# Kernel optimization log

Hardware: AMD Instinct MI355X
Metric: run time of the kernel (lower is better)

## Reference

```python
import jax, jax.numpy as jnp
import numpy as np

NUM_EXPERTS = 8
TOP_K = 2
ROUTED_SCALE = 1.0  # routed_scaling_factor
D_MODEL = 2048
D_FFN = 1408


def setup_inputs() -> dict:
    key = jax.random.key(0)
    ks = jax.random.split(key, 8)
    s = 0.02  # init scale for weights
    return {
        'hidden_states': jax.random.normal(ks[0], (2, 1024, D_MODEL), jnp.float32),
        'gate_w': jax.random.normal(ks[1], (NUM_EXPERTS, D_MODEL), jnp.float32) * s,
        'w_gate': jax.random.normal(ks[2], (NUM_EXPERTS, D_MODEL, D_FFN), jnp.float32) * s,
        'w_up': jax.random.normal(ks[3], (NUM_EXPERTS, D_MODEL, D_FFN), jnp.float32) * s,
        'w_down': jax.random.normal(ks[4], (NUM_EXPERTS, D_FFN, D_MODEL), jnp.float32) * s,
        'sw_gate': jax.random.normal(ks[5], (D_MODEL, D_FFN), jnp.float32) * s,
        'sw_up': jax.random.normal(ks[6], (D_MODEL, D_FFN), jnp.float32) * s,
        'sw_down': jax.random.normal(ks[7], (D_FFN, D_MODEL), jnp.float32) * s,
    }


def reference(hidden_states, gate_w, w_gate, w_up, w_down, sw_gate, sw_up, sw_down):
    B, S, D = hidden_states.shape
    x = hidden_states.reshape(-1, D)            # [T, D]
    T = x.shape[0]

    # --- router: fp32 linear -> softmax -> top-k -> renormalize ---
    logits = jnp.einsum('td,ed->te', x.astype(jnp.float32), gate_w)   # [T, E]
    probs = jax.nn.softmax(logits, axis=-1)
    topk_w, topk_ids = jax.lax.top_k(probs, TOP_K)                    # [T, K]
    topk_w = topk_w / jnp.sum(topk_w, axis=-1, keepdims=True)         # norm_topk_prob
    # dense per-token expert gates [T, E] (zero for unselected experts)
    gates = jnp.zeros((T, NUM_EXPERTS), jnp.float32).at[
        jnp.arange(T)[:, None], topk_ids].add(topk_w)
    gates = gates.astype(x.dtype)

    # --- routed experts: SwiGLU per expert, masked dense combine ---
    g = jnp.einsum('td,edf->etf', x, w_gate)    # [E, T, F]
    u = jnp.einsum('td,edf->etf', x, w_up)      # [E, T, F]
    h = jax.nn.silu(g) * u                      # SiluAndMul
    down = jnp.einsum('etf,efd->etd', h, w_down)  # [E, T, D]
    routed = jnp.einsum('te,etd->td', gates, down)  # combine
    routed = routed * ROUTED_SCALE

    # --- shared expert MLP ---
    shared = (jax.nn.silu(x @ sw_gate) * (x @ sw_up)) @ sw_down

    out = routed + shared
    return out.reshape(B, S, D)
```

## Files before the change

kernel.cpp:

```cpp
#include <hip/hip_runtime.h>
#include <hip/hip_bf16.h>

#define T_TOK 2048
#define DM    2048
#define FF    1408
#define NE    8
#define MT_ROUTED 40
#define MT_TOTAL  56
#define ROUTED_CAP 5120
#define NSLOT 7168

typedef unsigned short u16;
typedef __attribute__((ext_vector_type(4))) u16 u16x4;
typedef __attribute__((ext_vector_type(8))) short bf16x8;
typedef __attribute__((ext_vector_type(4))) float f32x4;

__device__ __forceinline__ u16 f2bf(float f) {
    unsigned u = __float_as_uint(f);
    unsigned r = (u + 0x7FFFu + ((u >> 16) & 1u)) >> 16;
    return (u16)r;
}
__device__ __forceinline__ float bf2f(u16 v) {
    return __uint_as_float(((unsigned)v) << 16);
}

__device__ __forceinline__ void gll16(const void* g, void* l) {
    __builtin_amdgcn_global_load_lds((const __attribute__((address_space(1))) void*)g,
                                     (__attribute__((address_space(3))) void*)l, 16, 0, 0);
}

constexpr size_t SZ_XB  = (size_t)T_TOK * DM * 2;
constexpr size_t SZ_WE  = (size_t)NE * DM * FF * 2;
constexpr size_t SZ_SW  = (size_t)DM * FF * 2;
constexpr size_t SZ_H   = (size_t)NSLOT * FF * 2;
constexpr size_t SZ_DN  = (size_t)NSLOT * DM * 2;

constexpr size_t OFF_XB   = 0;
constexpr size_t OFF_WGT  = OFF_XB + SZ_XB;
constexpr size_t OFF_WUT  = OFF_WGT + SZ_WE;
constexpr size_t OFF_WDT  = OFF_WUT + SZ_WE;
constexpr size_t OFF_SWG  = OFF_WDT + SZ_WE;
constexpr size_t OFF_SWU  = OFF_SWG + SZ_SW;
constexpr size_t OFF_SWD  = OFF_SWU + SZ_SW;
constexpr size_t OFF_H    = OFF_SWD + SZ_SW;
constexpr size_t OFF_DN   = OFF_H + SZ_H;
constexpr size_t OFF_TID  = OFF_DN + SZ_DN;
constexpr size_t OFF_TW   = OFF_TID + (size_t)T_TOK*2*4;
constexpr size_t OFF_PERM = OFF_TW  + (size_t)T_TOK*2*4;
constexpr size_t OFF_SW_S = OFF_PERM + (size_t)ROUTED_CAP*4;
constexpr size_t OFF_TKS  = OFF_SW_S + (size_t)ROUTED_CAP*4;
constexpr size_t OFF_TE   = OFF_TKS + (size_t)T_TOK*2*4;

__global__ void tcvtA_kernel(const float* __restrict__ wg, const float* __restrict__ wu,
                             const float* __restrict__ swg, const float* __restrict__ swu,
                             u16* __restrict__ wgT, u16* __restrict__ wuT,
                             u16* __restrict__ swgT, u16* __restrict__ swuT) {
    __shared__ u16 tile[64][72];
    const int z = blockIdx.z;
    const size_t msz = (size_t)DM * FF;
    const float* s; u16* d;
    if (z < 8)       { s = wg + (size_t)z * msz;        d = wgT + (size_t)z * msz; }
    else if (z < 16) { s = wu + (size_t)(z - 8) * msz;  d = wuT + (size_t)(z - 8) * msz; }
    else if (z == 16){ s = swg;                          d = swgT; }
    else             { s = swu;                          d = swuT; }
    const int R = DM, C = FF;
    const int r0 = blockIdx.y * 64, c0 = blockIdx.x * 64;
    const int tr = threadIdx.x >> 4, tc = (threadIdx.x & 15) * 4;
#pragma unroll
    for (int i = 0; i < 4; i++) {
        const int r = tr + i * 16;
        const float4 v = *(const float4*)(s + (size_t)(r0 + r) * C + (c0 + tc));
        tile[r][tc+0] = f2bf(v.x); tile[r][tc+1] = f2bf(v.y);
        tile[r][tc+2] = f2bf(v.z); tile[r][tc+3] = f2bf(v.w);
    }
    __syncthreads();
#pragma unroll
    for (int i = 0; i < 4; i++) {
        const int c = tr + i * 16;
        u16x4 o;
        o.x = tile[tc+0][c]; o.y = tile[tc+1][c]; o.z = tile[tc+2][c]; o.w = tile[tc+3][c];
        *(u16x4*)(d + (size_t)(c0 + c) * R + (r0 + tc)) = o;
    }
}

__global__ void tcvtB_kernel(const float* __restrict__ wd, const float* __restrict__ swd,
                             u16* __restrict__ wdT, u16* __restrict__ swdT) {
    __shared__ u16 tile[64][72];
    const int z = blockIdx.z;
    const size_t msz = (size_t)DM * FF;
    const float* s; u16* d;
    if (z < 8) { s = wd + (size_t)z * msz; d = wdT + (size_t)z * msz; }
    else       { s = swd;                  d = swdT; }
    const int R = FF, C = DM;
    const int r0 = blockIdx.y * 64, c0 = blockIdx.x * 64;
    const int tr = threadIdx.x >> 4, tc = (threadIdx.x & 15) * 4;
#pragma unroll
    for (int i = 0; i < 4; i++) {
        const int r = tr + i * 16;
        const float4 v = *(const float4*)(s + (size_t)(r0 + r) * C + (c0 + tc));
        tile[r][tc+0] = f2bf(v.x); tile[r][tc+1] = f2bf(v.y);
        tile[r][tc+2] = f2bf(v.z); tile[r][tc+3] = f2bf(v.w);
    }
    __syncthreads();
#pragma unroll
    for (int i = 0; i < 4; i++) {
        const int c = tr + i * 16;
        u16x4 o;
        o.x = tile[tc+0][c]; o.y = tile[tc+1][c]; o.z = tile[tc+2][c]; o.w = tile[tc+3][c];
        *(u16x4*)(d + (size_t)(c0 + c) * R + (r0 + tc)) = o;
    }
}

__global__ void router_kernel(const float* __restrict__ x, const float* __restrict__ gw,
                              u16* __restrict__ xb,
                              int* __restrict__ topk_id, float* __restrict__ topk_w) {
    const int wv = threadIdx.x >> 6, l = threadIdx.x & 63;
    const int t = blockIdx.x * 4 + wv;
    const float* xt = x + (size_t)t * DM;
    u16* xbt = xb + (size_t)t * DM;
    float acc[NE] = {0.f,0.f,0.f,0.f,0.f,0.f,0.f,0.f};
    for (int d = l * 4; d < DM; d += 256) {
        const float4 xv = *(const float4*)(xt + d);
        u16x4 o; o.x = f2bf(xv.x); o.y = f2bf(xv.y); o.z = f2bf(xv.z); o.w = f2bf(xv.w);
        *(u16x4*)(xbt + d) = o;
#pragma unroll
        for (int e = 0; e < NE; e++) {
            const float4 w4 = *(const float4*)(gw + e * DM + d);
            acc[e] += xv.x * w4.x + xv.y * w4.y + xv.z * w4.z + xv.w * w4.w;
        }
    }
#pragma unroll
    for (int e = 0; e < NE; e++)
#pragma unroll
        for (int off = 32; off > 0; off >>= 1) acc[e] += __shfl_xor(acc[e], off, 64);
    if (l == 0) {
        float m = acc[0];
#pragma unroll
        for (int e = 1; e < NE; e++) m = fmaxf(m, acc[e]);
        float p[NE];
#pragma unroll
        for (int e = 0; e < NE; e++) p[e] = __expf(acc[e] - m);
        int i1 = 0; float b1 = p[0];
#pragma unroll
        for (int e = 1; e < NE; e++) if (p[e] > b1) { b1 = p[e]; i1 = e; }
        int i2 = -1; float b2 = -1.f;
#pragma unroll
        for (int e = 0; e < NE; e++) if (e != i1 && p[e] > b2) { b2 = p[e]; i2 = e; }
        const float s = b1 + b2;
        topk_id[2*t] = i1; topk_id[2*t+1] = i2;
        topk_w[2*t] = b1 / s; topk_w[2*t+1] = b2 / s;
    }
}

__global__ void scan_kernel(const int* __restrict__ topk_id, const float* __restrict__ topk_w,
                            int* __restrict__ perm_token, float* __restrict__ slot_w,
                            int* __restrict__ tk_slot, int* __restrict__ tile_e) {
    const int e = blockIdx.x;
    const int tid = threadIdx.x;
    __shared__ int cnt[NE];
    __shared__ int tsum[256];
    int ids[16];
#pragma unroll
    for (int j = 0; j < 16; j++) ids[j] = topk_id[tid * 16 + j];
    if (tid < NE) cnt[tid] = 0;
    __syncthreads();
#pragma unroll
    for (int e2 = 0; e2 < NE; e2++) {
        int c = 0;
#pragma unroll
        for (int j = 0; j < 16; j++) c += (ids[j] == e2);
        if (c) atomicAdd(&cnt[e2], c);
    }
    int mySum = 0;
#pragma unroll
    for (int j = 0; j < 16; j++) mySum += (ids[j] == e);
    tsum[tid] = mySum;
    __syncthreads();
    if (tid == 0) { int run = 0; for (int i = 0; i < 256; i++) { int v = tsum[i]; tsum[i] = run; run += v; } }
    __syncthreads();
    int poff = 0;
#pragma unroll
    for (int e2 = 0; e2 < NE; e2++) { int p = (cnt[e2] + 127) & ~127; if (e2 < e) poff += p; }
    const int padded_e = (cnt[e] + 127) & ~127;
    int run = tsum[tid];
#pragma unroll
    for (int j = 0; j < 16; j++) {
        if (ids[j] == e) {
            const int i = tid * 16 + j;
            const int slot = poff + run;
            perm_token[slot] = i >> 1;
            slot_w[slot] = topk_w[i];
            tk_slot[i] = slot;
            run++;
        }
    }
    for (int r = cnt[e] + tid; r < padded_e; r += 256) { perm_token[poff + r] = 0; slot_w[poff + r] = 0.f; }
    if (tid == 0) for (int tt = poff >> 7; tt < (poff + padded_e) >> 7; tt++) tile_e[tt] = e;
    if (e == 0 && tid == 1) {
        int ptot = 0;
#pragma unroll
        for (int e2 = 0; e2 < NE; e2++) ptot += (cnt[e2] + 127) & ~127;
        for (int tt = ptot >> 7; tt < MT_ROUTED; tt++) tile_e[tt] = -1;
        for (int tt = MT_ROUTED; tt < MT_TOTAL; tt++) tile_e[tt] = 8;
    }
}

__global__ __launch_bounds__(256, 3)
void gemm1_kernel(const u16* __restrict__ xb,
                  const u16* __restrict__ wgT, const u16* __restrict__ wuT,
                  const u16* __restrict__ swgT, const u16* __restrict__ swuT,
                  const int* __restrict__ perm_token, const float* __restrict__ slot_w,
                  const int* __restrict__ tile_e, u16* __restrict__ hbuf) {
    const int mtile = blockIdx.y, ntile = blockIdx.x;
    const int e = tile_e[mtile];
    if (e < 0) return;
    __shared__ u16 lA[128 * 64], lB[128 * 64];
    __shared__ int lTok[128];
    __shared__ float lW[128];
    const int tid = threadIdx.x, l = tid & 63, w = tid >> 6;
    const bool sh = (e == 8);
    const int slot_base = sh ? (ROUTED_CAP + (mtile - MT_ROUTED) * 128) : mtile * 128;
    if (tid < 128) {
        if (sh) { lTok[tid] = (mtile - MT_ROUTED) * 128 + tid; lW[tid] = 1.0f; }
        else {
            int tok = perm_token[slot_base + tid];
            lTok[tid] = (tok < 0) ? 0 : tok;
            lW[tid] = slot_w[slot_base + tid];
        }
    }
    __syncthreads();
    const u16* Bg = sh ? swgT : (wgT + (size_t)e * FF * DM);
    const u16* Bu = sh ? swuT : (wuT + (size_t)e * FF * DM);
    const int n0 = ntile * 64;
    const u16* aSrc[4]; const u16* bSrc[4]; int ldsOff[4];
#pragma unroll
    for (int i = 0; i < 4; i++) {
        const int row = i * 32 + w * 8 + (l >> 3);
        const int ch = (l & 7) ^ (row & 7);
        ldsOff[i] = (i * 32 + w * 8) * 64;
        aSrc[i] = xb + (size_t)lTok[row] * DM + ch * 8;
        const u16* bbase = (i < 2) ? (Bg + (size_t)(n0 + row) * DM)
                                   : (Bu + (size_t)(n0 + row - 64) * DM);
        bSrc[i] = bbase + ch * 8;
    }
    f32x4 acc[2][8] = {};
    const int wm = w * 32;
    for (int k0 = 0; k0 < DM; k0 += 64) {
        __syncthreads();
#pragma unroll
        for (int i = 0; i < 4; i++) { gll16(aSrc[i] + k0, lA + ldsOff[i]); gll16(bSrc[i] + k0, lB + ldsOff[i]); }
        __syncthreads();
#pragma unroll
        for (int kk = 0; kk < 64; kk += 32) {
            bf16x8 af[2], bf_[8];
#pragma unroll
            for (int mi = 0; mi < 2; mi++) {
                const int row = wm + mi * 16 + (l & 15);
                const int ch = ((kk >> 3) + (l >> 4)) ^ (row & 7);
                af[mi] = *(const bf16x8*)(lA + row * 64 + ch * 8);
            }
#pragma unroll
            for (int ni = 0; ni < 8; ni++) {
                const int row = ni * 16 + (l & 15);
                const int ch = ((kk >> 3) + (l >> 4)) ^ (row & 7);
                bf_[ni] = *(const bf16x8*)(lB + row * 64 + ch * 8);
            }
#pragma unroll
            for (int mi = 0; mi < 2; mi++)
#pragma unroll
                for (int ni = 0; ni < 8; ni++)
                    acc[mi][ni] = __builtin_amdgcn_mfma_f32_16x16x32_bf16(af[mi], bf_[ni], acc[mi][ni], 0, 0, 0);
        }
    }
#pragma unroll
    for (int mi = 0; mi < 2; mi++)
#pragma unroll
        for (int r = 0; r < 4; r++) {
            const int m = wm + mi * 16 + (l >> 4) * 4 + r;
            const float wgt = lW[m];
#pragma unroll
            for (int ni = 0; ni < 4; ni++) {
                const int n = ni * 16 + (l & 15);
                const float g = acc[mi][ni][r], u = acc[mi][ni + 4][r];
                const float h = g * (1.f / (1.f + __expf(-g))) * u * wgt;
                hbuf[(size_t)(slot_base + m) * FF + n0 + n] = f2bf(h);
            }
        }
}

__global__ __launch_bounds__(256, 4)
void gemm2_kernel(const u16* __restrict__ hbuf, const u16* __restrict__ wdT,
                  const u16* __restrict__ swdT, const int* __restrict__ tile_e,
                  u16* __restrict__ dn) {
    const int mtile = blockIdx.y, ntile = blockIdx.x;
    const int e = tile_e[mtile];
    if (e < 0) return;
    __shared__ u16 lA[128 * 64], lB[64 * 64];
    const int tid = threadIdx.x, l = tid & 63, w = tid >> 6;
    const bool sh = (e == 8);
    const int slot_base = sh ? (ROUTED_CAP + (mtile - MT_ROUTED) * 128) : mtile * 128;
    const u16* Bp = sh ? swdT : (wdT + (size_t)e * DM * FF);
    const int n0 = ntile * 64;
    const u16* aSrc[4]; const u16* bSrc[2]; int ldsOffA[4]; int ldsOffB[2];
#pragma unroll
    for (int i = 0; i < 4; i++) {
        const int row = i * 32 + w * 8 + (l >> 3);
        const int ch = (l & 7) ^ (row & 7);
        ldsOffA[i] = (i * 32 + w * 8) * 64;
        aSrc[i] = hbuf + (size_t)(slot_base + row) * FF + ch * 8;
    }
#pragma unroll
    for (int i = 0; i < 2; i++) {
        const int row = i * 32 + w * 8 + (l >> 3);
        const int ch = (l & 7) ^ (row & 7);
        ldsOffB[i] = (i * 32 + w * 8) * 64;
        bSrc[i] = Bp + (size_t)(n0 + row) * FF + ch * 8;
    }
    f32x4 acc[2][4] = {};
    const int wm = w * 32;
    for (int k0 = 0; k0 < FF; k0 += 64) {
        __syncthreads();
#pragma unroll
        for (int i = 0; i < 4; i++) gll16(aSrc[i] + k0, lA + ldsOffA[i]);
#pragma unroll
        for (int i = 0; i < 2; i++) gll16(bSrc[i] + k0, lB + ldsOffB[i]);
        __syncthreads();
#pragma unroll
        for (int kk = 0; kk < 64; kk += 32) {
            bf16x8 af[2], bf_[4];
#pragma unroll
            for (int mi = 0; mi < 2; mi++) {
                const int row = wm + mi * 16 + (l & 15);
                const int ch = ((kk >> 3) + (l >> 4)) ^ (row & 7);
                af[mi] = *(const bf16x8*)(lA + row * 64 + ch * 8);
            }
#pragma unroll
            for (int ni = 0; ni < 4; ni++) {
                const int row = ni * 16 + (l & 15);
                const int ch = ((kk >> 3) + (l >> 4)) ^ (row & 7);
                bf_[ni] = *(const bf16x8*)(lB + row * 64 + ch * 8);
            }
#pragma unroll
            for (int mi = 0; mi < 2; mi++)
#pragma unroll
                for (int ni = 0; ni < 4; ni++)
                    acc[mi][ni] = __builtin_amdgcn_mfma_f32_16x16x32_bf16(af[mi], bf_[ni], acc[mi][ni], 0, 0, 0);
        }
    }
#pragma unroll
    for (int mi = 0; mi < 2; mi++)
#pragma unroll
        for (int r = 0; r < 4; r++) {
            const int m = wm + mi * 16 + (l >> 4) * 4 + r;
#pragma unroll
            for (int ni = 0; ni < 4; ni++) {
                const int n = ni * 16 + (l & 15);
                dn[(size_t)(slot_base + m) * DM + n0 + n] = f2bf(acc[mi][ni][r]);
            }
        }
}

__global__ void combine_kernel(const u16* __restrict__ dn, const int* __restrict__ tk_slot,
                               float* __restrict__ out) {
    const int i = blockIdx.x * 256 + threadIdx.x;
    const int base = i * 8;
    const int t = base >> 11, d = base & 2047;
    const int s1 = tk_slot[2 * t], s2 = tk_slot[2 * t + 1];
    const bf16x8 a = *(const bf16x8*)(dn + (size_t)s1 * DM + d);
    const bf16x8 b = *(const bf16x8*)(dn + (size_t)s2 * DM + d);
    const bf16x8 c = *(const bf16x8*)(dn + (size_t)(ROUTED_CAP + t) * DM + d);
    float o[8];
#pragma unroll
    for (int j = 0; j < 8; j++)
        o[j] = bf2f((u16)a[j]) + bf2f((u16)b[j]) + bf2f((u16)c[j]);
    float4 lo, hi;
    lo.x = o[0]; lo.y = o[1]; lo.z = o[2]; lo.w = o[3];
    hi.x = o[4]; hi.y = o[5]; hi.z = o[6]; hi.w = o[7];
    *(float4*)(out + base) = lo;
    *(float4*)(out + base + 4) = hi;
}

extern "C" void kernel_launch(void* const* d_in, const int* in_sizes, int n_in,
                              void* d_out, int out_size, void* d_ws, size_t ws_size,
                              hipStream_t stream) {
    (void)in_sizes; (void)n_in; (void)out_size; (void)ws_size;
    const float* x   = (const float*)d_in[0];
    const float* gw  = (const float*)d_in[1];
    const float* wg  = (const float*)d_in[2];
    const float* wu  = (const float*)d_in[3];
    const float* wd  = (const float*)d_in[4];
    const float* swg = (const float*)d_in[5];
    const float* swu = (const float*)d_in[6];
    const float* swd = (const float*)d_in[7];
    float* out = (float*)d_out;
    char* ws = (char*)d_ws;

    u16*   xb    = (u16*)(ws + OFF_XB);
    u16*   wgT   = (u16*)(ws + OFF_WGT);
    u16*   wuT   = (u16*)(ws + OFF_WUT);
    u16*   wdT   = (u16*)(ws + OFF_WDT);
    u16*   swgT  = (u16*)(ws + OFF_SWG);
    u16*   swuT  = (u16*)(ws + OFF_SWU);
    u16*   swdT  = (u16*)(ws + OFF_SWD);
    u16*   hbuf  = (u16*)(ws + OFF_H);
    u16*   dn    = (u16*)(ws + OFF_DN);
    int*   tid_  = (int*)(ws + OFF_TID);
    float* tw    = (float*)(ws + OFF_TW);
    int*   perm  = (int*)(ws + OFF_PERM);
    float* slw   = (float*)(ws + OFF_SW_S);
    int*   tks   = (int*)(ws + OFF_TKS);
    int*   te    = (int*)(ws + OFF_TE);

    router_kernel<<<T_TOK / 4, 256, 0, stream>>>(x, gw, xb, tid_, tw);
    scan_kernel<<<NE, 256, 0, stream>>>(tid_, tw, perm, slw, tks, te);
    tcvtA_kernel<<<dim3(FF / 64, DM / 64, 18), 256, 0, stream>>>(wg, wu, swg, swu, wgT, wuT, swgT, swuT);
    tcvtB_kernel<<<dim3(DM / 64, FF / 64, 9), 256, 0, stream>>>(wd, swd, wdT, swdT);
    gemm1_kernel<<<dim3(FF / 64, MT_TOTAL), 256, 0, stream>>>(xb, wgT, wuT, swgT, swuT, perm, slw, te, hbuf);
    gemm2_kernel<<<dim3(DM / 64, MT_TOTAL), 256, 0, stream>>>(hbuf, wdT, swdT, te, dn);
    combine_kernel<<<(T_TOK * DM / 8) / 256, 256, 0, stream>>>(dn, tks, out);
}
```

Before: 293.4 us.

## Enlarge GEMM M-tiles to 256 rows with 512-thread blocks and 2D warp split

Expert-sorted token tiles are padded to 256 rows instead of 128, and both GEMM kernels now run 512-thread blocks with a 2D warp layout. GEMM2 also widens its N tile to 128. The larger tiles cut how often weights are reloaded per token and raise MFMA work per LDS load. In exchange there is more padding waste per expert, fewer blocks in the grid (possibly under-filling the CUs), and more LDS and register pressure per block.

After: 401.6 us. +36.9%, slower.

```diff
diff --git a/kernel.cpp b/kernel.cpp
--- a/kernel.cpp
+++ b/kernel.cpp
@@ -5,10 +5,11 @@
 #define DM    2048
 #define FF    1408
 #define NE    8
-#define MT_ROUTED 40
-#define MT_TOTAL  56
-#define ROUTED_CAP 5120
-#define NSLOT 7168
+#define BMT   256
+#define MT_ROUTED 24
+#define MT_TOTAL  32
+#define ROUTED_CAP 6144
+#define NSLOT 8192
 
 typedef unsigned short u16;
 typedef __attribute__((ext_vector_type(4))) u16 u16x4;
@@ -180,8 +181,8 @@
     __syncthreads();
     int poff = 0;
 #pragma unroll
-    for (int e2 = 0; e2 < NE; e2++) { int p = (cnt[e2] + 127) & ~127; if (e2 < e) poff += p; }
-    const int padded_e = (cnt[e] + 127) & ~127;
+    for (int e2 = 0; e2 < NE; e2++) { int p = (cnt[e2] + 255) & ~255; if (e2 < e) poff += p; }
+    const int padded_e = (cnt[e] + 255) & ~255;
     int run = tsum[tid];
 #pragma unroll
     for (int j = 0; j < 16; j++) {
@@ -195,17 +196,17 @@
         }
     }
     for (int r = cnt[e] + tid; r < padded_e; r += 256) { perm_token[poff + r] = 0; slot_w[poff + r] = 0.f; }
-    if (tid == 0) for (int tt = poff >> 7; tt < (poff + padded_e) >> 7; tt++) tile_e[tt] = e;
+    if (tid == 0) for (int tt = poff >> 8; tt < (poff + padded_e) >> 8; tt++) tile_e[tt] = e;
     if (e == 0 && tid == 1) {
         int ptot = 0;
 #pragma unroll
-        for (int e2 = 0; e2 < NE; e2++) ptot += (cnt[e2] + 127) & ~127;
-        for (int tt = ptot >> 7; tt < MT_ROUTED; tt++) tile_e[tt] = -1;
+        for (int e2 = 0; e2 < NE; e2++) ptot += (cnt[e2] + 255) & ~255;
+        for (int tt = ptot >> 8; tt < MT_ROUTED; tt++) tile_e[tt] = -1;
         for (int tt = MT_ROUTED; tt < MT_TOTAL; tt++) tile_e[tt] = 8;
     }
 }
 
-__global__ __launch_bounds__(256, 3)
+__global__ __launch_bounds__(512, 4)
 void gemm1_kernel(const u16* __restrict__ xb,
                   const u16* __restrict__ wgT, const u16* __restrict__ wuT,
                   const u16* __restrict__ swgT, const u16* __restrict__ swuT,
@@ -214,147 +215,154 @@
     const int mtile = blockIdx.y, ntile = blockIdx.x;
     const int e = tile_e[mtile];
     if (e < 0) return;
-    __shared__ u16 lA[128 * 64], lB[128 * 64];
-    __shared__ int lTok[128];
-    __shared__ float lW[128];
+    __shared__ u16 lA[256 * 64], lB[128 * 64];
+    __shared__ int lTok[256];
+    __shared__ float lW[256];
     const int tid = threadIdx.x, l = tid & 63, w = tid >> 6;
     const bool sh = (e == 8);
-    const int slot_base = sh ? (ROUTED_CAP + (mtile - MT_ROUTED) * 128) : mtile * 128;
-    if (tid < 128) {
-        if (sh) { lTok[tid] = (mtile - MT_ROUTED) * 128 + tid; lW[tid] = 1.0f; }
-        else {
-            int tok = perm_token[slot_base + tid];
-            lTok[tid] = (tok < 0) ? 0 : tok;
-            lW[tid] = slot_w[slot_base + tid];
-        }
+    const int slot_base = sh ? (ROUTED_CAP + (mtile - MT_ROUTED) * BMT) : mtile * BMT;
+    if (tid < 256) {
+        if (sh) { lTok[tid] = (mtile - MT_ROUTED) * BMT + tid; lW[tid] = 1.0f; }
+        else    { lTok[tid] = perm_token[slot_base + tid]; lW[tid] = slot_w[slot_base + tid]; }
     }
     __syncthreads();
     const u16* Bg = sh ? swgT : (wgT + (size_t)e * FF * DM);
     const u16* Bu = sh ? swuT : (wuT + (size_t)e * FF * DM);
     const int n0 = ntile * 64;
-    const u16* aSrc[4]; const u16* bSrc[4]; int ldsOff[4];
-#pragma unroll
-    for (int i = 0; i < 4; i++) {
-        const int row = i * 32 + w * 8 + (l >> 3);
+    const u16* aSrc[4]; const u16* bSrc[2]; int aOff[4], bOff[2];
+#pragma unroll
+    for (int i = 0; i < 4; i++) {
+        const int row = i * 64 + w * 8 + (l >> 3);
         const int ch = (l & 7) ^ (row & 7);
-        ldsOff[i] = (i * 32 + w * 8) * 64;
+        aOff[i] = (i * 64 + w * 8) * 64;
         aSrc[i] = xb + (size_t)lTok[row] * DM + ch * 8;
-        const u16* bbase = (i < 2) ? (Bg + (size_t)(n0 + row) * DM)
-                                   : (Bu + (size_t)(n0 + row - 64) * DM);
+    }
+#pragma unroll
+    for (int i = 0; i < 2; i++) {
+        const int row = i * 64 + w * 8 + (l >> 3);
+        const int ch = (l & 7) ^ (row & 7);
+        bOff[i] = (i * 64 + w * 8) * 64;
+        const u16* bbase = (i == 0) ? (Bg + (size_t)(n0 + row) * DM)
+                                    : (Bu + (size_t)(n0 + row - 64) * DM);
         bSrc[i] = bbase + ch * 8;
     }
-    f32x4 acc[2][8] = {};
-    const int wm = w * 32;
+    f32x4 accg[4][2] = {}; f32x4 accu[4][2] = {};
+    const int wm = (w >> 1) * 64, wn = (w & 1) * 32;
     for (int k0 = 0; k0 < DM; k0 += 64) {
         __syncthreads();
 #pragma unroll
-        for (int i = 0; i < 4; i++) { gll16(aSrc[i] + k0, lA + ldsOff[i]); gll16(bSrc[i] + k0, lB + ldsOff[i]); }
+        for (int i = 0; i < 4; i++) gll16(aSrc[i] + k0, lA + aOff[i]);
+#pragma unroll
+        for (int i = 0; i < 2; i++) gll16(bSrc[i] + k0, lB + bOff[i]);
         __syncthreads();
 #pragma unroll
         for (int kk = 0; kk < 64; kk += 32) {
-            bf16x8 af[2], bf_[8];
-#pragma unroll
-            for (int mi = 0; mi < 2; mi++) {
+            bf16x8 af[4], bgf[2], buf2[2];
+#pragma unroll
+            for (int mi = 0; mi < 4; mi++) {
                 const int row = wm + mi * 16 + (l & 15);
                 const int ch = ((kk >> 3) + (l >> 4)) ^ (row & 7);
                 af[mi] = *(const bf16x8*)(lA + row * 64 + ch * 8);
             }
 #pragma unroll
-            for (int ni = 0; ni < 8; ni++) {
-                const int row = ni * 16 + (l & 15);
-                const int ch = ((kk >> 3) + (l >> 4)) ^ (row & 7);
-                bf_[ni] = *(const bf16x8*)(lB + row * 64 + ch * 8);
-            }
-#pragma unroll
-            for (int mi = 0; mi < 2; mi++)
-#pragma unroll
-                for (int ni = 0; ni < 8; ni++)
-                    acc[mi][ni] = __builtin_amdgcn_mfma_f32_16x16x32_bf16(af[mi], bf_[ni], acc[mi][ni], 0, 0, 0);
-        }
-    }
-#pragma unroll
-    for (int mi = 0; mi < 2; mi++)
+            for (int ni = 0; ni < 2; ni++) {
+                const int rowg = wn + ni * 16 + (l & 15);
+                const int ch = ((kk >> 3) + (l >> 4)) ^ (rowg & 7);
+                bgf[ni]  = *(const bf16x8*)(lB + rowg * 64 + ch * 8);
+                buf2[ni] = *(const bf16x8*)(lB + (rowg + 64) * 64 + ch * 8);
+            }
+#pragma unroll
+            for (int mi = 0; mi < 4; mi++)
+#pragma unroll
+                for (int ni = 0; ni < 2; ni++) {
+                    accg[mi][ni] = __builtin_amdgcn_mfma_f32_16x16x32_bf16(af[mi], bgf[ni], accg[mi][ni], 0, 0, 0);
+                    accu[mi][ni] = __builtin_amdgcn_mfma_f32_16x16x32_bf16(af[mi], buf2[ni], accu[mi][ni], 0, 0, 0);
+                }
+        }
+    }
+#pragma unroll
+    for (int mi = 0; mi < 4; mi++)
 #pragma unroll
         for (int r = 0; r < 4; r++) {
             const int m = wm + mi * 16 + (l >> 4) * 4 + r;
             const float wgt = lW[m];
 #pragma unroll
-            for (int ni = 0; ni < 4; ni++) {
-                const int n = ni * 16 + (l & 15);
-                const float g = acc[mi][ni][r], u = acc[mi][ni + 4][r];
+            for (int ni = 0; ni < 2; ni++) {
+                const int n = wn + ni * 16 + (l & 15);
+                const float g = accg[mi][ni][r], u = accu[mi][ni][r];
                 const float h = g * (1.f / (1.f + __expf(-g))) * u * wgt;
                 hbuf[(size_t)(slot_base + m) * FF + n0 + n] = f2bf(h);
             }
         }
 }
 
-__global__ __launch_bounds__(256, 4)
+__global__ __launch_bounds__(512, 4)
 void gemm2_kernel(const u16* __restrict__ hbuf, const u16* __restrict__ wdT,
                   const u16* __restrict__ swdT, const int* __restrict__ tile_e,
                   u16* __restrict__ dn) {
     const int mtile = blockIdx.y, ntile = blockIdx.x;
     const int e = tile_e[mtile];
     if (e < 0) return;
-    __shared__ u16 lA[128 * 64], lB[64 * 64];
+    __shared__ u16 lA[256 * 64], lB[128 * 64];
     const int tid = threadIdx.x, l = tid & 63, w = tid >> 6;
     const bool sh = (e == 8);
-    const int slot_base = sh ? (ROUTED_CAP + (mtile - MT_ROUTED) * 128) : mtile * 128;
+    const int slot_base = sh ? (ROUTED_CAP + (mtile - MT_ROUTED) * BMT) : mtile * BMT;
     const u16* Bp = sh ? swdT : (wdT + (size_t)e * DM * FF);
-    const int n0 = ntile * 64;
-    const u16* aSrc[4]; const u16* bSrc[2]; int ldsOffA[4]; int ldsOffB[2];
-#pragma unroll
-    for (int i = 0; i < 4; i++) {
-        const int row = i * 32 + w * 8 + (l >> 3);
+    const int n0 = ntile * 128;
+    const u16* aSrc[4]; const u16* bSrc[2]; int aOff[4], bOff[2];
+#pragma unroll
+    for (int i = 0; i < 4; i++) {
+        const int row = i * 64 + w * 8 + (l >> 3);
         const int ch = (l & 7) ^ (row & 7);
-        ldsOffA[i] = (i * 32 + w * 8) * 64;
+        aOff[i] = (i * 64 + w * 8) * 64;
         aSrc[i] = hbuf + (size_t)(slot_base + row) * FF + ch * 8;
     }
 #pragma unroll
     for (int i = 0; i < 2; i++) {
-        const int row = i * 32 + w * 8 + (l >> 3);
+        const int row = i * 64 + w * 8 + (l >> 3);
         const int ch = (l & 7) ^ (row & 7);
-        ldsOffB[i] = (i * 32 + w * 8) * 64;
+        bOff[i] = (i * 64 + w * 8) * 64;
         bSrc[i] = Bp + (size_t)(n0 + row) * FF + ch * 8;
     }
-    f32x4 acc[2][4] = {};
-    const int wm = w * 32;
+    f32x4 acc[4][4] = {};
+    const int wm = (w >> 1) * 64, wn = (w & 1) * 64;
     for (int k0 = 0; k0 < FF; k0 += 64) {
         __syncthreads();
 #pragma unroll
-        for (int i = 0; i < 4; i++) gll16(aSrc[i] + k0, lA + ldsOffA[i]);
-#pragma unroll
-        for (int i = 0; i < 2; i++) gll16(bSrc[i] + k0, lB + ldsOffB[i]);
+        for (int i = 0; i < 4; i++) gll16(aSrc[i] + k0, lA + aOff[i]);
+#pragma unroll
+        for (int i = 0; i < 2; i++) gll16(bSrc[i] + k0, lB + bOff[i]);
         __syncthreads();
 #pragma unroll
         for (int kk = 0; kk < 64; kk += 32) {
-            bf16x8 af[2], bf_[4];
-#pragma unroll
-            for (int mi = 0; mi < 2; mi++) {
+            bf16x8 af[4], bf_[4];
+#pragma unroll
+            for (int mi = 0; mi < 4; mi++) {
                 const int row = wm + mi * 16 + (l & 15);
                 const int ch = ((kk >> 3) + (l >> 4)) ^ (row & 7);
                 af[mi] = *(const bf16x8*)(lA + row * 64 + ch * 8);
             }
 #pragma unroll
             for (int ni = 0; ni < 4; ni++) {
-                const int row = ni * 16 + (l & 15);
+                const int row = wn + ni * 16 + (l & 15);
                 const int ch = ((kk >> 3) + (l >> 4)) ^ (row & 7);
                 bf_[ni] = *(const bf16x8*)(lB + row * 64 + ch * 8);
             }
 #pragma unroll
-            for (int mi = 0; mi < 2; mi++)
+            for (int mi = 0; mi < 4; mi++)
 #pragma unroll
                 for (int ni = 0; ni < 4; ni++)
                     acc[mi][ni] = __builtin_amdgcn_mfma_f32_16x16x32_bf16(af[mi], bf_[ni], acc[mi][ni], 0, 0, 0);
         }
     }
 #pragma unroll
-    for (int mi = 0; mi < 2; mi++)
+    for (int mi = 0; mi < 4; mi++)
 #pragma unroll
         for (int r = 0; r < 4; r++) {
             const int m = wm + mi * 16 + (l >> 4) * 4 + r;
 #pragma unroll
             for (int ni = 0; ni < 4; ni++) {
-                const int n = ni * 16 + (l & 15);
+                const int n = wn + ni * 16 + (l & 15);
                 dn[(size_t)(slot_base + m) * DM + n0 + n] = f2bf(acc[mi][ni][r]);
             }
         }
@@ -415,7 +423,7 @@
     scan_kernel<<<NE, 256, 0, stream>>>(tid_, tw, perm, slw, tks, te);
     tcvtA_kernel<<<dim3(FF / 64, DM / 64, 18), 256, 0, stream>>>(wg, wu, swg, swu, wgT, wuT, swgT, swuT);
     tcvtB_kernel<<<dim3(DM / 64, FF / 64, 9), 256, 0, stream>>>(wd, swd, wdT, swdT);
-    gemm1_kernel<<<dim3(FF / 64, MT_TOTAL), 256, 0, stream>>>(xb, wgT, wuT, swgT, swuT, perm, slw, te, hbuf);
-    gemm2_kernel<<<dim3(DM / 64, MT_TOTAL), 256, 0, stream>>>(hbuf, wdT, swdT, te, dn);
+    gemm1_kernel<<<dim3(FF / 64, MT_TOTAL), 512, 0, stream>>>(xb, wgT, wuT, swgT, swuT, perm, slw, te, hbuf);
+    gemm2_kernel<<<dim3(DM / 128, MT_TOTAL), 512, 0, stream>>>(hbuf, wdT, swdT, te, dn);
     combine_kernel<<<(T_TOK * DM / 8) / 256, 256, 0, stream>>>(dn, tks, out);
 }
```

## Double-buffer GEMM LDS tiles, swizzle block order, merge weight transpose kernels

Applied to the files above, without the earlier changes.

Both expert GEMMs now keep two LDS buffers and prefetch the next K-slice with async global-to-LDS loads while computing the current one, replacing the two-barrier load-then-compute loop. Blocks get a 1-D launch with an XCD-aware swizzle so tiles sharing a weight slice land together. The two weight transpose/convert kernels become one launch. The cost is doubled LDS, lower occupancy bounds, and a dropped guard on negative token indices.

Result: slower. 343.7 us (+17.1%).

```diff
diff --git a/kernel.cpp b/kernel.cpp
--- a/kernel.cpp
+++ b/kernel.cpp
@@ -51,48 +51,30 @@
 constexpr size_t OFF_TKS  = OFF_SW_S + (size_t)ROUTED_CAP*4;
 constexpr size_t OFF_TE   = OFF_TKS + (size_t)T_TOK*2*4;
 
-__global__ void tcvtA_kernel(const float* __restrict__ wg, const float* __restrict__ wu,
-                             const float* __restrict__ swg, const float* __restrict__ swu,
-                             u16* __restrict__ wgT, u16* __restrict__ wuT,
-                             u16* __restrict__ swgT, u16* __restrict__ swuT) {
+__global__ void tcvt_kernel(const float* __restrict__ wg, const float* __restrict__ wu,
+                            const float* __restrict__ swg, const float* __restrict__ swu,
+                            const float* __restrict__ wd, const float* __restrict__ swd,
+                            u16* __restrict__ wgT, u16* __restrict__ wuT,
+                            u16* __restrict__ swgT, u16* __restrict__ swuT,
+                            u16* __restrict__ wdT, u16* __restrict__ swdT) {
     __shared__ u16 tile[64][72];
     const int z = blockIdx.z;
     const size_t msz = (size_t)DM * FF;
-    const float* s; u16* d;
-    if (z < 8)       { s = wg + (size_t)z * msz;        d = wgT + (size_t)z * msz; }
-    else if (z < 16) { s = wu + (size_t)(z - 8) * msz;  d = wuT + (size_t)(z - 8) * msz; }
-    else if (z == 16){ s = swg;                          d = swgT; }
-    else             { s = swu;                          d = swuT; }
-    const int R = DM, C = FF;
-    const int r0 = blockIdx.y * 64, c0 = blockIdx.x * 64;
-    const int tr = threadIdx.x >> 4, tc = (threadIdx.x & 15) * 4;
-#pragma unroll
-    for (int i = 0; i < 4; i++) {
-        const int r = tr + i * 16;
-        const float4 v = *(const float4*)(s + (size_t)(r0 + r) * C + (c0 + tc));
-        tile[r][tc+0] = f2bf(v.x); tile[r][tc+1] = f2bf(v.y);
-        tile[r][tc+2] = f2bf(v.z); tile[r][tc+3] = f2bf(v.w);
-    }
-    __syncthreads();
-#pragma unroll
-    for (int i = 0; i < 4; i++) {
-        const int c = tr + i * 16;
-        u16x4 o;
-        o.x = tile[tc+0][c]; o.y = tile[tc+1][c]; o.z = tile[tc+2][c]; o.w = tile[tc+3][c];
-        *(u16x4*)(d + (size_t)(c0 + c) * R + (r0 + tc)) = o;
-    }
-}
-
-__global__ void tcvtB_kernel(const float* __restrict__ wd, const float* __restrict__ swd,
-                             u16* __restrict__ wdT, u16* __restrict__ swdT) {
-    __shared__ u16 tile[64][72];
-    const int z = blockIdx.z;
-    const size_t msz = (size_t)DM * FF;
-    const float* s; u16* d;
-    if (z < 8) { s = wd + (size_t)z * msz; d = wdT + (size_t)z * msz; }
-    else       { s = swd;                  d = swdT; }
-    const int R = FF, C = DM;
-    const int r0 = blockIdx.y * 64, c0 = blockIdx.x * 64;
+    const float* s; u16* d; int R, C, trow, tcol;
+    if (z < 18) {
+        R = DM; C = FF;
+        trow = blockIdx.x / 22; tcol = blockIdx.x % 22;
+        if (z < 8)       { s = wg + (size_t)z * msz;       d = wgT + (size_t)z * msz; }
+        else if (z < 16) { s = wu + (size_t)(z - 8) * msz; d = wuT + (size_t)(z - 8) * msz; }
+        else if (z == 16){ s = swg;                         d = swgT; }
+        else             { s = swu;                         d = swuT; }
+    } else {
+        R = FF; C = DM;
+        trow = blockIdx.x / 32; tcol = blockIdx.x % 32;
+        if (z < 26) { s = wd + (size_t)(z - 18) * msz; d = wdT + (size_t)(z - 18) * msz; }
+        else        { s = swd;                          d = swdT; }
+    }
+    const int r0 = trow * 64, c0 = tcol * 64;
     const int tr = threadIdx.x >> 4, tc = (threadIdx.x & 15) * 4;
 #pragma unroll
     for (int i = 0; i < 4; i++) {
@@ -205,16 +187,18 @@
     }
 }
 
-__global__ __launch_bounds__(256, 3)
+__global__ __launch_bounds__(256, 2)
 void gemm1_kernel(const u16* __restrict__ xb,
                   const u16* __restrict__ wgT, const u16* __restrict__ wuT,
                   const u16* __restrict__ swgT, const u16* __restrict__ swuT,
                   const int* __restrict__ perm_token, const float* __restrict__ slot_w,
                   const int* __restrict__ tile_e, u16* __restrict__ hbuf) {
-    const int mtile = blockIdx.y, ntile = blockIdx.x;
+    const int bid = blockIdx.x;
+    const int swz = (bid & 7) * 154 + (bid >> 3);
+    const int mtile = swz % 56, ntile = swz / 56;
     const int e = tile_e[mtile];
     if (e < 0) return;
-    __shared__ u16 lA[128 * 64], lB[128 * 64];
+    __shared__ u16 lA[2][128 * 64], lB[2][128 * 64];
     __shared__ int lTok[128];
     __shared__ float lW[128];
     const int tid = threadIdx.x, l = tid & 63, w = tid >> 6;
@@ -222,11 +206,7 @@
     const int slot_base = sh ? (ROUTED_CAP + (mtile - MT_ROUTED) * 128) : mtile * 128;
     if (tid < 128) {
         if (sh) { lTok[tid] = (mtile - MT_ROUTED) * 128 + tid; lW[tid] = 1.0f; }
-        else {
-            int tok = perm_token[slot_base + tid];
-            lTok[tid] = (tok < 0) ? 0 : tok;
-            lW[tid] = slot_w[slot_base + tid];
-        }
+        else    { lTok[tid] = perm_token[slot_base + tid]; lW[tid] = slot_w[slot_base + tid]; }
     }
     __syncthreads();
     const u16* Bg = sh ? swgT : (wgT + (size_t)e * FF * DM);
@@ -245,11 +225,15 @@
     }
     f32x4 acc[2][8] = {};
     const int wm = w * 32;
-    for (int k0 = 0; k0 < DM; k0 += 64) {
-        __syncthreads();
-#pragma unroll
-        for (int i = 0; i < 4; i++) { gll16(aSrc[i] + k0, lA + ldsOff[i]); gll16(bSrc[i] + k0, lB + ldsOff[i]); }
-        __syncthreads();
+
+    auto stage = [&](int buf, int k0) {
+#pragma unroll
+        for (int i = 0; i < 4; i++) {
+            gll16(aSrc[i] + k0, lA[buf] + ldsOff[i]);
+            gll16(bSrc[i] + k0, lB[buf] + ldsOff[i]);
+        }
+    };
+    auto compute = [&](int buf) {
 #pragma unroll
         for (int kk = 0; kk < 64; kk += 32) {
             bf16x8 af[2], bf_[8];
@@ -257,13 +241,13 @@
             for (int mi = 0; mi < 2; mi++) {
                 const int row = wm + mi * 16 + (l & 15);
                 const int ch = ((kk >> 3) + (l >> 4)) ^ (row & 7);
-                af[mi] = *(const bf16x8*)(lA + row * 64 + ch * 8);
+                af[mi] = *(const bf16x8*)(lA[buf] + row * 64 + ch * 8);
             }
 #pragma unroll
             for (int ni = 0; ni < 8; ni++) {
                 const int row = ni * 16 + (l & 15);
                 const int ch = ((kk >> 3) + (l >> 4)) ^ (row & 7);
-                bf_[ni] = *(const bf16x8*)(lB + row * 64 + ch * 8);
+                bf_[ni] = *(const bf16x8*)(lB[buf] + row * 64 + ch * 8);
             }
 #pragma unroll
             for (int mi = 0; mi < 2; mi++)
@@ -271,7 +255,21 @@
                 for (int ni = 0; ni < 8; ni++)
                     acc[mi][ni] = __builtin_amdgcn_mfma_f32_16x16x32_bf16(af[mi], bf_[ni], acc[mi][ni], 0, 0, 0);
         }
-    }
+    };
+
+    stage(0, 0);
+    for (int t = 0; t < 31; t++) {
+        const int cur = t & 1;
+        stage(cur ^ 1, (t + 1) * 64);
+        asm volatile("s_waitcnt vmcnt(8)" ::: "memory");
+        __builtin_amdgcn_s_barrier();
+        compute(cur);
+        __builtin_amdgcn_s_barrier();
+    }
+    asm volatile("s_waitcnt vmcnt(0)" ::: "memory");
+    __builtin_amdgcn_s_barrier();
+    compute(1);
+
 #pragma unroll
     for (int mi = 0; mi < 2; mi++)
 #pragma unroll
@@ -288,43 +286,46 @@
         }
 }
 
-__global__ __launch_bounds__(256, 4)
+__global__ __launch_bounds__(256, 3)
 void gemm2_kernel(const u16* __restrict__ hbuf, const u16* __restrict__ wdT,
                   const u16* __restrict__ swdT, const int* __restrict__ tile_e,
                   u16* __restrict__ dn) {
-    const int mtile = blockIdx.y, ntile = blockIdx.x;
+    const int bid = blockIdx.x;
+    const int swz = (bid & 7) * 224 + (bid >> 3);
+    const int mtile = swz % 56, ntile = swz / 56;
     const int e = tile_e[mtile];
     if (e < 0) return;
-    __shared__ u16 lA[128 * 64], lB[64 * 64];
+    __shared__ u16 lA[2][128 * 64], lB[2][64 * 64];
     const int tid = threadIdx.x, l = tid & 63, w = tid >> 6;
     const bool sh = (e == 8);
     const int slot_base = sh ? (ROUTED_CAP + (mtile - MT_ROUTED) * 128) : mtile * 128;
     const u16* Bp = sh ? swdT : (wdT + (size_t)e * DM * FF);
     const int n0 = ntile * 64;
-    const u16* aSrc[4]; const u16* bSrc[2]; int ldsOffA[4]; int ldsOffB[2];
+    const u16* aSrc[4]; const u16* bSrc[2]; int aOff[4], bOff[2];
 #pragma unroll
     for (int i = 0; i < 4; i++) {
         const int row = i * 32 + w * 8 + (l >> 3);
         const int ch = (l & 7) ^ (row & 7);
-        ldsOffA[i] = (i * 32 + w * 8) * 64;
+        aOff[i] = (i * 32 + w * 8) * 64;
         aSrc[i] = hbuf + (size_t)(slot_base + row) * FF + ch * 8;
     }
 #pragma unroll
     for (int i = 0; i < 2; i++) {
         const int row = i * 32 + w * 8 + (l >> 3);
         const int ch = (l & 7) ^ (row & 7);
-        ldsOffB[i] = (i * 32 + w * 8) * 64;
+        bOff[i] = (i * 32 + w * 8) * 64;
         bSrc[i] = Bp + (size_t)(n0 + row) * FF + ch * 8;
     }
     f32x4 acc[2][4] = {};
     const int wm = w * 32;
-    for (int k0 = 0; k0 < FF; k0 += 64) {
-        __syncthreads();
-#pragma unroll
-        for (int i = 0; i < 4; i++) gll16(aSrc[i] + k0, lA + ldsOffA[i]);
-#pragma unroll
-        for (int i = 0; i < 2; i++) gll16(bSrc[i] + k0, lB + ldsOffB[i]);
-        __syncthreads();
+
+    auto stage = [&](int buf, int k0) {
+#pragma unroll
+        for (int i = 0; i < 4; i++) gll16(aSrc[i] + k0, lA[buf] + aOff[i]);
+#pragma unroll
+        for (int i = 0; i < 2; i++) gll16(bSrc[i] + k0, lB[buf] + bOff[i]);
+    };
+    auto compute = [&](int buf) {
 #pragma unroll
         for (int kk = 0; kk < 64; kk += 32) {
             bf16x8 af[2], bf_[4];
@@ -332,13 +333,13 @@
             for (int mi = 0; mi < 2; mi++) {
                 const int row = wm + mi * 16 + (l & 15);
                 const int ch = ((kk >> 3) + (l >> 4)) ^ (row & 7);
-                af[mi] = *(const bf16x8*)(lA + row * 64 + ch * 8);
+                af[mi] = *(const bf16x8*)(lA[buf] + row * 64 + ch * 8);
             }
 #pragma unroll
             for (int ni = 0; ni < 4; ni++) {
                 const int row = ni * 16 + (l & 15);
                 const int ch = ((kk >> 3) + (l >> 4)) ^ (row & 7);
-                bf_[ni] = *(const bf16x8*)(lB + row * 64 + ch * 8);
+                bf_[ni] = *(const bf16x8*)(lB[buf] + row * 64 + ch * 8);
             }
 #pragma unroll
             for (int mi = 0; mi < 2; mi++)
@@ -346,7 +347,21 @@
                 for (int ni = 0; ni < 4; ni++)
                     acc[mi][ni] = __builtin_amdgcn_mfma_f32_16x16x32_bf16(af[mi], bf_[ni], acc[mi][ni], 0, 0, 0);
         }
-    }
+    };
+
+    stage(0, 0);
+    for (int t = 0; t < 21; t++) {
+        const int cur = t & 1;
+        stage(cur ^ 1, (t + 1) * 64);
+        asm volatile("s_waitcnt vmcnt(6)" ::: "memory");
+        __builtin_amdgcn_s_barrier();
+        compute(cur);
+        __builtin_amdgcn_s_barrier();
+    }
+    asm volatile("s_waitcnt vmcnt(0)" ::: "memory");
+    __builtin_amdgcn_s_barrier();
+    compute(1);
+
 #pragma unroll
     for (int mi = 0; mi < 2; mi++)
 #pragma unroll
@@ -413,9 +428,9 @@
 
     router_kernel<<<T_TOK / 4, 256, 0, stream>>>(x, gw, xb, tid_, tw);
     scan_kernel<<<NE, 256, 0, stream>>>(tid_, tw, perm, slw, tks, te);
-    tcvtA_kernel<<<dim3(FF / 64, DM / 64, 18), 256, 0, stream>>>(wg, wu, swg, swu, wgT, wuT, swgT, swuT);
-    tcvtB_kernel<<<dim3(DM / 64, FF / 64, 9), 256, 0, stream>>>(wd, swd, wdT, swdT);
-    gemm1_kernel<<<dim3(FF / 64, MT_TOTAL), 256, 0, stream>>>(xb, wgT, wuT, swgT, swuT, perm, slw, te, hbuf);
-    gemm2_kernel<<<dim3(DM / 64, MT_TOTAL), 256, 0, stream>>>(hbuf, wdT, swdT, te, dn);
+    tcvt_kernel<<<dim3(704, 1, 27), 256, 0, stream>>>(wg, wu, swg, swu, wd, swd,
+                                                      wgT, wuT, swgT, swuT, wdT, swdT);
+    gemm1_kernel<<<1232, 256, 0, stream>>>(xb, wgT, wuT, swgT, swuT, perm, slw, te, hbuf);
+    gemm2_kernel<<<1792, 256, 0, stream>>>(hbuf, wdT, swdT, te, dn);
     combine_kernel<<<(T_TOK * DM / 8) / 256, 256, 0, stream>>>(dn, tks, out);
 }
```
